# Kernel tuning notes

Hardware: AMD Instinct MI355X
Metric: run time of the kernel (lower is better)

Reference implementation:

```python
import jax, jax.numpy as jnp
import numpy as np

H, W = 4096, 4096
MIN_VAL, MAX_VAL = 0, 256
D = MAX_VAL - MIN_VAL - 1  # 255 candidate thresholds t = 0..254
N_BINS = MAX_VAL           # pixel values live in [0, 256)


def setup_inputs() -> dict:
    key = jax.random.key(0)
    img = jax.random.randint(key, (H, W), MIN_VAL, MAX_VAL, dtype=jnp.int32)
    return {"img_HxW": img}


def reference(img_HxW):
    hw = H * W
    flat = img_HxW.ravel()
    # Histogram of pixel counts and pixel-value sums (float32 accumulation,
    # matching torch.sum(..., dtype=torch.float32) in the original).
    cnt = jax.ops.segment_sum(jnp.ones_like(flat, jnp.float32), flat, num_segments=N_BINS)
    val_sum = jax.ops.segment_sum(flat.astype(jnp.float32), flat, num_segments=N_BINS)
    # Cumulative sums give, for each threshold t, the count/sum of pixels <= t.
    # This equals the original's broadcast compare + masked sum over [H*W, d].
    num_b = jnp.cumsum(cnt)[:D]        # pixels in class "black" (<= t)
    sum_b = jnp.cumsum(val_sum)[:D]    # sum of those pixels
    num_w = hw - num_b                  # pixels in class "white" (> t)
    sum_w = jnp.sum(val_sum) - sum_b
    mean_b = sum_b / num_b
    mean_w = sum_w / num_w
    var_hist = num_b * num_w * (mean_b - mean_w) ** 2  # inter-class variance
    thresh = jnp.argmax(var_hist).astype(jnp.int32)
    bin_img = jnp.where(img_HxW <= thresh,
                        jnp.int32(MIN_VAL), jnp.int32(MAX_VAL))
    return thresh, bin_img
```

## Files before the change

kernel.cpp:

```cpp
#include <hip/hip_runtime.h>

#define HW_TOTAL (4096 * 4096)
#define NBINS 256
#define NCHUNK (HW_TOTAL / 4)
#define HIST_B 512
#define BLK 1024
#define BATCH 8

typedef int int4n __attribute__((ext_vector_type(4)));
typedef int int4a __attribute__((ext_vector_type(4), aligned(4)));

#define WS_NEED (HIST_B * NBINS * 4 + 256)

template <int MODE>
__global__ __launch_bounds__(BLK, 8) void otsu_hist_k(const int4* __restrict__ img4,
                                                      unsigned* __restrict__ out) {
    __shared__ unsigned h[4 * NBINS];
    const int t = threadIdx.x;
    for (int i = t; i < 4 * NBINS; i += BLK) h[i] = 0;
    __syncthreads();

    unsigned* hp = h + (t & 3);
    const int wave = t >> 6, lane = t & 63;
    const int i0 = blockIdx.x * (BLK * BATCH) + wave * (64 * BATCH) + lane;

    int4 v[BATCH];
#pragma unroll
    for (int k = 0; k < BATCH; ++k) v[k] = img4[i0 + k * 64];
#pragma unroll
    for (int k = 0; k < BATCH; ++k) {
        atomicAdd(&hp[((unsigned)v[k].x) << 2], 1u);
        atomicAdd(&hp[((unsigned)v[k].y) << 2], 1u);
        atomicAdd(&hp[((unsigned)v[k].z) << 2], 1u);
        atomicAdd(&hp[((unsigned)v[k].w) << 2], 1u);
    }
    __syncthreads();

    if (t < NBINS) {
        unsigned s = h[t << 2] + h[(t << 2) | 1] + h[(t << 2) | 2] + h[(t << 2) | 3];
        if (MODE == 0) {
            out[blockIdx.x * NBINS + t] = s;
        } else {
            if (s) atomicAdd(&out[t], s);
        }
    }
}

__global__ __launch_bounds__(1024) void otsu_thresh_k(const unsigned* __restrict__ partials,
                                                      int B,
                                                      int* __restrict__ d_out,
                                                      int* __restrict__ thresh_ws) {
    __shared__ unsigned red[4][NBINS];
    __shared__ unsigned cnt[NBINS];

    const int bin = threadIdx.x & 255;
    const int q = threadIdx.x >> 8;
    const int BQ = (B + 3) / 4;
    int r = q * BQ;
    const int e = min((q + 1) * BQ, B);
    unsigned s = 0;
    for (; r + 16 <= e; r += 16) {
#pragma unroll
        for (int k = 0; k < 16; ++k) s += partials[(r + k) * NBINS + bin];
    }
    for (; r < e; ++r) s += partials[r * NBINS + bin];
    red[q][bin] = s;
    __syncthreads();

    if (threadIdx.x < NBINS)
        cnt[bin] = red[0][bin] + red[1][bin] + red[2][bin] + red[3][bin];
    __syncthreads();

    if (threadIdx.x >= 64) return;
    const int lane = threadIdx.x;

    uint4 c4 = ((const uint4*)cnt)[lane];
    unsigned cs[4] = {c4.x, c4.y, c4.z, c4.w};

    unsigned long long lc[4], lv[4];
    unsigned long long ccum = 0ull, vcum = 0ull;
#pragma unroll
    for (int k = 0; k < 4; ++k) {
        ccum += cs[k];
        vcum += (unsigned long long)cs[k] * (unsigned)(4 * lane + k);
        lc[k] = ccum;
        lv[k] = vcum;
    }
    unsigned long long cscan = ccum, vscan = vcum;
    for (int d = 1; d < 64; d <<= 1) {
        unsigned long long cu = __shfl_up(cscan, d);
        unsigned long long vu = __shfl_up(vscan, d);
        if (lane >= d) { cscan += cu; vscan += vu; }
    }
    const unsigned long long cbase = cscan - ccum;
    const unsigned long long vbase = vscan - vcum;
    const unsigned long long vtotal = __shfl(vscan, 63);

    double best = -1.0;
    int bestt = 255;
    const double hw = (double)HW_TOTAL;
    const double vtot_d = (double)vtotal;
#pragma unroll
    for (int k = 0; k < 4; ++k) {
        int tt = 4 * lane + k;
        if (tt > 254) continue;
        double nb = (double)(cbase + lc[k]);
        double sb = (double)(vbase + lv[k]);
        double nw = hw - nb;
        double sw = vtot_d - sb;
        double dm = sb / nb - sw / nw;
        double var = nb * nw * dm * dm;
        if (var > best || (var == best && tt < bestt)) { best = var; bestt = tt; }
    }
    for (int d = 32; d >= 1; d >>= 1) {
        double ov = __shfl_xor(best, d);
        int ot = __shfl_xor(bestt, d);
        if (ov > best || (ov == best && ot < bestt)) { best = ov; bestt = ot; }
    }
    if (lane == 0) {
        d_out[0] = bestt;
        *thresh_ws = bestt;
    }
}

__global__ __launch_bounds__(BLK, 8) void otsu_bin_k(const int* __restrict__ img,
                                                     int* __restrict__ out,
                                                     const int* __restrict__ thresh_ws) {
    const int thresh = *thresh_ws;
    const int t = threadIdx.x;
    const int wave = t >> 6, lane = t & 63;
    const int i0 = blockIdx.x * (BLK * BATCH) + wave * (64 * BATCH) + lane;

#pragma unroll
    for (int k = 0; k < BATCH; ++k) {
        const int c = i0 + k * 64;
        const int4a* vp = (const int4a*)(img + (c ? 4 * c - 1 : 0));
        int4a v = *vp;
        int4n o;
        o.x = (v.x <= thresh) ? 0 : 256;
        o.y = (v.y <= thresh) ? 0 : 256;
        o.z = (v.z <= thresh) ? 0 : 256;
        o.w = (v.w <= thresh) ? 0 : 256;
        if (c == 0) {
            o.w = o.z; o.z = o.y; o.y = o.x; o.x = thresh;
        }
        *((int4n*)out + c) = o;
    }
    if (i0 == 0)
        out[HW_TOTAL] = (img[HW_TOTAL - 1] <= thresh) ? 0 : 256;
}

extern "C" void kernel_launch(void* const* d_in, const int* in_sizes, int n_in,
                              void* d_out, int out_size, void* d_ws, size_t ws_size,
                              hipStream_t stream) {
    const int* img = (const int*)d_in[0];
    int* out = (int*)d_out;
    int* thresh_ws = (int*)d_ws;
    unsigned* hist_buf = (unsigned*)((char*)d_ws + 256);

    if (ws_size >= (size_t)WS_NEED) {
        otsu_hist_k<0><<<HIST_B, BLK, 0, stream>>>((const int4*)img, hist_buf);
        otsu_thresh_k<<<1, 1024, 0, stream>>>(hist_buf, HIST_B, out, thresh_ws);
    } else {
        (void)hipMemsetAsync(hist_buf, 0, NBINS * sizeof(unsigned), stream);
        otsu_hist_k<1><<<HIST_B, BLK, 0, stream>>>((const int4*)img, hist_buf);
        otsu_thresh_k<<<1, 1024, 0, stream>>>(hist_buf, 1, out, thresh_ws);
    }
    otsu_bin_k<<<HIST_B, BLK, 0, stream>>>(img, out, thresh_ws);
}
```

Measured before the change: 44.24 us.

## Fuse histogram, threshold and binarize into one persistent kernel with grid barrier

```diff
diff --git a/kernel.cpp b/kernel.cpp
--- a/kernel.cpp
+++ b/kernel.cpp
@@ -3,88 +3,192 @@
 #define HW_TOTAL (4096 * 4096)
 #define NBINS 256
 #define NCHUNK (HW_TOTAL / 4)
-#define HIST_B 512
+#define GRID_B 256
 #define BLK 1024
-#define BATCH 8
+#define BATCH 16
+#define HALF 8
 
 typedef int int4n __attribute__((ext_vector_type(4)));
 typedef int int4a __attribute__((ext_vector_type(4), aligned(4)));
 
-#define WS_NEED (HIST_B * NBINS * 4 + 256)
-
-template <int MODE>
-__global__ __launch_bounds__(BLK, 8) void otsu_hist_k(const int4* __restrict__ img4,
-                                                      unsigned* __restrict__ out) {
+#define WS_WORDS 258
+#define WS_NEED (WS_WORDS * 4)
+
+__global__ __launch_bounds__(BLK, 4) void otsu_fused_k(const int* __restrict__ img,
+                                                       int* __restrict__ out,
+                                                       unsigned* __restrict__ ws) {
+    __shared__ unsigned h[4 * NBINS];
+    __shared__ int s_thresh;
+    __shared__ unsigned s_islast;
+
+    const int t = threadIdx.x;
+    const int b = blockIdx.x;
+    const int4* img4 = (const int4*)img;
+
+    for (int i = t; i < 4 * NBINS; i += BLK) h[i] = 0;
+    __syncthreads();
+
+    unsigned* hp = h + (t & 3);
+    const int wave = t >> 6, lane = t & 63;
+    const int i0 = b * (BLK * BATCH) + wave * (64 * BATCH) + lane;
+
+#pragma unroll
+    for (int half = 0; half < BATCH / HALF; ++half) {
+        int4 v[HALF];
+        const int j0 = i0 + half * (HALF * 64);
+#pragma unroll
+        for (int k = 0; k < HALF; ++k) v[k] = img4[j0 + k * 64];
+#pragma unroll
+        for (int k = 0; k < HALF; ++k) {
+            atomicAdd(&hp[((unsigned)v[k].x) << 2], 1u);
+            atomicAdd(&hp[((unsigned)v[k].y) << 2], 1u);
+            atomicAdd(&hp[((unsigned)v[k].z) << 2], 1u);
+            atomicAdd(&hp[((unsigned)v[k].w) << 2], 1u);
+        }
+    }
+    __syncthreads();
+
+    if (t < NBINS) {
+        unsigned s = h[t << 2] + h[(t << 2) | 1] + h[(t << 2) | 2] + h[(t << 2) | 3];
+        atomicAdd(&ws[t], s);
+    }
+    __syncthreads();
+
+    if (t == 0) {
+        __threadfence();
+        unsigned my = __hip_atomic_fetch_add(&ws[256], 1u, __ATOMIC_ACQ_REL,
+                                             __HIP_MEMORY_SCOPE_AGENT);
+        s_islast = (my == GRID_B - 1) ? 1u : 0u;
+    }
+    __syncthreads();
+
+    if (s_islast) {
+        if (t < NBINS)
+            h[t] = __hip_atomic_load(&ws[t], __ATOMIC_RELAXED, __HIP_MEMORY_SCOPE_AGENT);
+        __syncthreads();
+        if (t < 64) {
+            uint4 c4 = ((const uint4*)h)[t];
+            unsigned cs[4] = {c4.x, c4.y, c4.z, c4.w};
+
+            unsigned long long lc[4], lv[4];
+            unsigned long long ccum = 0ull, vcum = 0ull;
+#pragma unroll
+            for (int k = 0; k < 4; ++k) {
+                ccum += cs[k];
+                vcum += (unsigned long long)cs[k] * (unsigned)(4 * t + k);
+                lc[k] = ccum;
+                lv[k] = vcum;
+            }
+            unsigned long long cscan = ccum, vscan = vcum;
+            for (int d = 1; d < 64; d <<= 1) {
+                unsigned long long cu = __shfl_up(cscan, d);
+                unsigned long long vu = __shfl_up(vscan, d);
+                if (t >= d) { cscan += cu; vscan += vu; }
+            }
+            const unsigned long long cbase = cscan - ccum;
+            const unsigned long long vbase = vscan - vcum;
+            const unsigned long long vtotal = __shfl(vscan, 63);
+
+            double best = -1.0;
+            int bestt = 255;
+            const double hw = (double)HW_TOTAL;
+            const double vtot_d = (double)vtotal;
+#pragma unroll
+            for (int k = 0; k < 4; ++k) {
+                int tt = 4 * t + k;
+                if (tt > 254) continue;
+                double nb = (double)(cbase + lc[k]);
+                double sb = (double)(vbase + lv[k]);
+                double nw = hw - nb;
+                double sw = vtot_d - sb;
+                double dm = sb / nb - sw / nw;
+                double var = nb * nw * dm * dm;
+                if (var > best || (var == best && tt < bestt)) { best = var; bestt = tt; }
+            }
+            for (int d = 32; d >= 1; d >>= 1) {
+                double ov = __shfl_xor(best, d);
+                int ot = __shfl_xor(bestt, d);
+                if (ov > best || (ov == best && ot < bestt)) { best = ov; bestt = ot; }
+            }
+            if (t == 0) {
+                out[0] = bestt;
+                s_thresh = bestt;
+                __hip_atomic_store(&ws[257], (unsigned)bestt + 1u, __ATOMIC_RELEASE,
+                                   __HIP_MEMORY_SCOPE_AGENT);
+            }
+        }
+    } else if (t == 0) {
+        unsigned f;
+        while ((f = __hip_atomic_load(&ws[257], __ATOMIC_ACQUIRE,
+                                      __HIP_MEMORY_SCOPE_AGENT)) == 0u)
+            __builtin_amdgcn_s_sleep(8);
+        s_thresh = (int)f - 1;
+    }
+    __syncthreads();
+    const int thresh = s_thresh;
+
+#pragma unroll
+    for (int half = 0; half < BATCH / HALF; ++half) {
+        const int j0 = i0 + half * (HALF * 64);
+#pragma unroll
+        for (int k = 0; k < HALF; ++k) {
+            const int c = j0 + k * 64;
+            int4a v = *(const int4a*)(img + (c ? 4 * c - 1 : 0));
+            int4n o;
+            o.x = (v.x <= thresh) ? 0 : 256;
+            o.y = (v.y <= thresh) ? 0 : 256;
+            o.z = (v.z <= thresh) ? 0 : 256;
+            o.w = (v.w <= thresh) ? 0 : 256;
+            if (c == 0) { o.w = o.z; o.z = o.y; o.y = o.x; o.x = thresh; }
+            __builtin_nontemporal_store(o, (int4n*)out + c);
+        }
+    }
+    if (i0 == 0)
+        out[HW_TOTAL] = (img[HW_TOTAL - 1] <= thresh) ? 0 : 256;
+}
+
+__global__ __launch_bounds__(BLK, 4) void fb_hist_k(const int4* __restrict__ img4,
+                                                    unsigned* __restrict__ ghist) {
     __shared__ unsigned h[4 * NBINS];
     const int t = threadIdx.x;
     for (int i = t; i < 4 * NBINS; i += BLK) h[i] = 0;
     __syncthreads();
-
     unsigned* hp = h + (t & 3);
     const int wave = t >> 6, lane = t & 63;
     const int i0 = blockIdx.x * (BLK * BATCH) + wave * (64 * BATCH) + lane;
-
-    int4 v[BATCH];
-#pragma unroll
-    for (int k = 0; k < BATCH; ++k) v[k] = img4[i0 + k * 64];
-#pragma unroll
-    for (int k = 0; k < BATCH; ++k) {
-        atomicAdd(&hp[((unsigned)v[k].x) << 2], 1u);
-        atomicAdd(&hp[((unsigned)v[k].y) << 2], 1u);
-        atomicAdd(&hp[((unsigned)v[k].z) << 2], 1u);
-        atomicAdd(&hp[((unsigned)v[k].w) << 2], 1u);
-    }
-    __syncthreads();
-
+#pragma unroll
+    for (int half = 0; half < BATCH / HALF; ++half) {
+        int4 v[HALF];
+        const int j0 = i0 + half * (HALF * 64);
+#pragma unroll
+        for (int k = 0; k < HALF; ++k) v[k] = img4[j0 + k * 64];
+#pragma unroll
+        for (int k = 0; k < HALF; ++k) {
+            atomicAdd(&hp[((unsigned)v[k].x) << 2], 1u);
+            atomicAdd(&hp[((unsigned)v[k].y) << 2], 1u);
+            atomicAdd(&hp[((unsigned)v[k].z) << 2], 1u);
+            atomicAdd(&hp[((unsigned)v[k].w) << 2], 1u);
+        }
+    }
+    __syncthreads();
     if (t < NBINS) {
         unsigned s = h[t << 2] + h[(t << 2) | 1] + h[(t << 2) | 2] + h[(t << 2) | 3];
-        if (MODE == 0) {
-            out[blockIdx.x * NBINS + t] = s;
-        } else {
-            if (s) atomicAdd(&out[t], s);
-        }
-    }
-}
-
-__global__ __launch_bounds__(1024) void otsu_thresh_k(const unsigned* __restrict__ partials,
-                                                      int B,
-                                                      int* __restrict__ d_out,
-                                                      int* __restrict__ thresh_ws) {
-    __shared__ unsigned red[4][NBINS];
-    __shared__ unsigned cnt[NBINS];
-
-    const int bin = threadIdx.x & 255;
-    const int q = threadIdx.x >> 8;
-    const int BQ = (B + 3) / 4;
-    int r = q * BQ;
-    const int e = min((q + 1) * BQ, B);
-    unsigned s = 0;
-    for (; r + 16 <= e; r += 16) {
-#pragma unroll
-        for (int k = 0; k < 16; ++k) s += partials[(r + k) * NBINS + bin];
-    }
-    for (; r < e; ++r) s += partials[r * NBINS + bin];
-    red[q][bin] = s;
-    __syncthreads();
-
-    if (threadIdx.x < NBINS)
-        cnt[bin] = red[0][bin] + red[1][bin] + red[2][bin] + red[3][bin];
-    __syncthreads();
-
-    if (threadIdx.x >= 64) return;
+        if (s) atomicAdd(&ghist[t], s);
+    }
+}
+
+__global__ __launch_bounds__(64) void fb_thresh_k(const unsigned* __restrict__ cnt,
+                                                  int* __restrict__ d_out,
+                                                  unsigned* __restrict__ ws) {
     const int lane = threadIdx.x;
-
     uint4 c4 = ((const uint4*)cnt)[lane];
     unsigned cs[4] = {c4.x, c4.y, c4.z, c4.w};
-
-    unsigned long long lc[4], lv[4];
-    unsigned long long ccum = 0ull, vcum = 0ull;
+    unsigned long long lc[4], lv[4], ccum = 0ull, vcum = 0ull;
 #pragma unroll
     for (int k = 0; k < 4; ++k) {
         ccum += cs[k];
         vcum += (unsigned long long)cs[k] * (unsigned)(4 * lane + k);
-        lc[k] = ccum;
-        lv[k] = vcum;
+        lc[k] = ccum; lv[k] = vcum;
     }
     unsigned long long cscan = ccum, vscan = vcum;
     for (int d = 1; d < 64; d <<= 1) {
@@ -92,22 +196,15 @@
         unsigned long long vu = __shfl_up(vscan, d);
         if (lane >= d) { cscan += cu; vscan += vu; }
     }
-    const unsigned long long cbase = cscan - ccum;
-    const unsigned long long vbase = vscan - vcum;
+    const unsigned long long cbase = cscan - ccum, vbase = vscan - vcum;
     const unsigned long long vtotal = __shfl(vscan, 63);
-
-    double best = -1.0;
-    int bestt = 255;
-    const double hw = (double)HW_TOTAL;
-    const double vtot_d = (double)vtotal;
+    double best = -1.0; int bestt = 255;
 #pragma unroll
     for (int k = 0; k < 4; ++k) {
         int tt = 4 * lane + k;
         if (tt > 254) continue;
-        double nb = (double)(cbase + lc[k]);
-        double sb = (double)(vbase + lv[k]);
-        double nw = hw - nb;
-        double sw = vtot_d - sb;
+        double nb = (double)(cbase + lc[k]), sb = (double)(vbase + lv[k]);
+        double nw = (double)HW_TOTAL - nb, sw = (double)vtotal - sb;
         double dm = sb / nb - sw / nw;
         double var = nb * nw * dm * dm;
         if (var > best || (var == best && tt < bestt)) { best = var; bestt = tt; }
@@ -117,34 +214,31 @@
         int ot = __shfl_xor(bestt, d);
         if (ov > best || (ov == best && ot < bestt)) { best = ov; bestt = ot; }
     }
-    if (lane == 0) {
-        d_out[0] = bestt;
-        *thresh_ws = bestt;
-    }
-}
-
-__global__ __launch_bounds__(BLK, 8) void otsu_bin_k(const int* __restrict__ img,
-                                                     int* __restrict__ out,
-                                                     const int* __restrict__ thresh_ws) {
-    const int thresh = *thresh_ws;
+    if (lane == 0) { d_out[0] = bestt; ws[257] = (unsigned)bestt + 1u; }
+}
+
+__global__ __launch_bounds__(BLK, 4) void fb_bin_k(const int* __restrict__ img,
+                                                   int* __restrict__ out,
+                                                   const unsigned* __restrict__ ws) {
+    const int thresh = (int)ws[257] - 1;
     const int t = threadIdx.x;
     const int wave = t >> 6, lane = t & 63;
     const int i0 = blockIdx.x * (BLK * BATCH) + wave * (64 * BATCH) + lane;
-
-#pragma unroll
-    for (int k = 0; k < BATCH; ++k) {
-        const int c = i0 + k * 64;
-        const int4a* vp = (const int4a*)(img + (c ? 4 * c - 1 : 0));
-        int4a v = *vp;
-        int4n o;
-        o.x = (v.x <= thresh) ? 0 : 256;
-        o.y = (v.y <= thresh) ? 0 : 256;
-        o.z = (v.z <= thresh) ? 0 : 256;
-        o.w = (v.w <= thresh) ? 0 : 256;
-        if (c == 0) {
-            o.w = o.z; o.z = o.y; o.y = o.x; o.x = thresh;
-        }
-        *((int4n*)out + c) = o;
+#pragma unroll
+    for (int half = 0; half < BATCH / HALF; ++half) {
+        const int j0 = i0 + half * (HALF * 64);
+#pragma unroll
+        for (int k = 0; k < HALF; ++k) {
+            const int c = j0 + k * 64;
+            int4a v = *(const int4a*)(img + (c ? 4 * c - 1 : 0));
+            int4n o;
+            o.x = (v.x <= thresh) ? 0 : 256;
+            o.y = (v.y <= thresh) ? 0 : 256;
+            o.z = (v.z <= thresh) ? 0 : 256;
+            o.w = (v.w <= thresh) ? 0 : 256;
+            if (c == 0) { o.w = o.z; o.z = o.y; o.y = o.x; o.x = thresh; }
+            __builtin_nontemporal_store(o, (int4n*)out + c);
+        }
     }
     if (i0 == 0)
         out[HW_TOTAL] = (img[HW_TOTAL - 1] <= thresh) ? 0 : 256;
@@ -155,16 +249,15 @@
                               hipStream_t stream) {
     const int* img = (const int*)d_in[0];
     int* out = (int*)d_out;
-    int* thresh_ws = (int*)d_ws;
-    unsigned* hist_buf = (unsigned*)((char*)d_ws + 256);
+    unsigned* ws = (unsigned*)d_ws;
+
+    (void)hipMemsetAsync(ws, 0, WS_NEED, stream);
 
     if (ws_size >= (size_t)WS_NEED) {
-        otsu_hist_k<0><<<HIST_B, BLK, 0, stream>>>((const int4*)img, hist_buf);
-        otsu_thresh_k<<<1, 1024, 0, stream>>>(hist_buf, HIST_B, out, thresh_ws);
+        otsu_fused_k<<<GRID_B, BLK, 0, stream>>>(img, out, ws);
     } else {
-        (void)hipMemsetAsync(hist_buf, 0, NBINS * sizeof(unsigned), stream);
-        otsu_hist_k<1><<<HIST_B, BLK, 0, stream>>>((const int4*)img, hist_buf);
-        otsu_thresh_k<<<1, 1024, 0, stream>>>(hist_buf, 1, out, thresh_ws);
-    }
-    otsu_bin_k<<<HIST_B, BLK, 0, stream>>>(img, out, thresh_ws);
-}
+        fb_hist_k<<<GRID_B, BLK, 0, stream>>>((const int4*)img, ws);
+        fb_thresh_k<<<1, 64, 0, stream>>>(ws, out, ws);
+        fb_bin_k<<<GRID_B, BLK, 0, stream>>>(img, out, ws);
+    }
+}
```

Measured after the change: 77.89 us. +76.1%, slower.

## Fuse threshold computation into binarize kernel, use global atomic histogram

Applied to the files above, without the earlier changes.

```diff
diff --git a/kernel.cpp b/kernel.cpp
--- a/kernel.cpp
+++ b/kernel.cpp
@@ -3,77 +3,16 @@
 #define HW_TOTAL (4096 * 4096)
 #define NBINS 256
 #define NCHUNK (HW_TOTAL / 4)
-#define HIST_B 512
+#define GRID_B 512
 #define BLK 1024
 #define BATCH 8
 
 typedef int int4n __attribute__((ext_vector_type(4)));
 typedef int int4a __attribute__((ext_vector_type(4), aligned(4)));
 
-#define WS_NEED (HIST_B * NBINS * 4 + 256)
+#define WS_NEED (NBINS * 4)
 
-template <int MODE>
-__global__ __launch_bounds__(BLK, 8) void otsu_hist_k(const int4* __restrict__ img4,
-                                                      unsigned* __restrict__ out) {
-    __shared__ unsigned h[4 * NBINS];
-    const int t = threadIdx.x;
-    for (int i = t; i < 4 * NBINS; i += BLK) h[i] = 0;
-    __syncthreads();
-
-    unsigned* hp = h + (t & 3);
-    const int wave = t >> 6, lane = t & 63;
-    const int i0 = blockIdx.x * (BLK * BATCH) + wave * (64 * BATCH) + lane;
-
-    int4 v[BATCH];
-#pragma unroll
-    for (int k = 0; k < BATCH; ++k) v[k] = img4[i0 + k * 64];
-#pragma unroll
-    for (int k = 0; k < BATCH; ++k) {
-        atomicAdd(&hp[((unsigned)v[k].x) << 2], 1u);
-        atomicAdd(&hp[((unsigned)v[k].y) << 2], 1u);
-        atomicAdd(&hp[((unsigned)v[k].z) << 2], 1u);
-        atomicAdd(&hp[((unsigned)v[k].w) << 2], 1u);
-    }
-    __syncthreads();
-
-    if (t < NBINS) {
-        unsigned s = h[t << 2] + h[(t << 2) | 1] + h[(t << 2) | 2] + h[(t << 2) | 3];
-        if (MODE == 0) {
-            out[blockIdx.x * NBINS + t] = s;
-        } else {
-            if (s) atomicAdd(&out[t], s);
-        }
-    }
-}
-
-__global__ __launch_bounds__(1024) void otsu_thresh_k(const unsigned* __restrict__ partials,
-                                                      int B,
-                                                      int* __restrict__ d_out,
-                                                      int* __restrict__ thresh_ws) {
-    __shared__ unsigned red[4][NBINS];
-    __shared__ unsigned cnt[NBINS];
-
-    const int bin = threadIdx.x & 255;
-    const int q = threadIdx.x >> 8;
-    const int BQ = (B + 3) / 4;
-    int r = q * BQ;
-    const int e = min((q + 1) * BQ, B);
-    unsigned s = 0;
-    for (; r + 16 <= e; r += 16) {
-#pragma unroll
-        for (int k = 0; k < 16; ++k) s += partials[(r + k) * NBINS + bin];
-    }
-    for (; r < e; ++r) s += partials[r * NBINS + bin];
-    red[q][bin] = s;
-    __syncthreads();
-
-    if (threadIdx.x < NBINS)
-        cnt[bin] = red[0][bin] + red[1][bin] + red[2][bin] + red[3][bin];
-    __syncthreads();
-
-    if (threadIdx.x >= 64) return;
-    const int lane = threadIdx.x;
-
+__device__ __forceinline__ int otsu_scan64(const unsigned* cnt, int lane) {
     uint4 c4 = ((const uint4*)cnt)[lane];
     unsigned cs[4] = {c4.x, c4.y, c4.z, c4.w};
 
@@ -117,34 +56,67 @@
         int ot = __shfl_xor(bestt, d);
         if (ov > best || (ov == best && ot < bestt)) { best = ov; bestt = ot; }
     }
-    if (lane == 0) {
-        d_out[0] = bestt;
-        *thresh_ws = bestt;
+    return bestt;
+}
+
+__global__ __launch_bounds__(BLK, 8) void otsu_hist_k(const int4* __restrict__ img4,
+                                                      unsigned* __restrict__ ghist) {
+    __shared__ unsigned h[4 * NBINS];
+    const int t = threadIdx.x;
+    for (int i = t; i < 4 * NBINS; i += BLK) h[i] = 0;
+    __syncthreads();
+
+    unsigned* hp = h + (t & 3);
+    const int wave = t >> 6, lane = t & 63;
+    const int i0 = blockIdx.x * (BLK * BATCH) + wave * (64 * BATCH) + lane;
+
+    int4 v[BATCH];
+#pragma unroll
+    for (int k = 0; k < BATCH; ++k) v[k] = img4[i0 + k * 64];
+#pragma unroll
+    for (int k = 0; k < BATCH; ++k) {
+        atomicAdd(&hp[((unsigned)v[k].x) << 2], 1u);
+        atomicAdd(&hp[((unsigned)v[k].y) << 2], 1u);
+        atomicAdd(&hp[((unsigned)v[k].z) << 2], 1u);
+        atomicAdd(&hp[((unsigned)v[k].w) << 2], 1u);
+    }
+    __syncthreads();
+
+    if (t < NBINS) {
+        unsigned s = h[t << 2] + h[(t << 2) | 1] + h[(t << 2) | 2] + h[(t << 2) | 3];
+        if (s) atomicAdd(&ghist[t], s);
     }
 }
 
 __global__ __launch_bounds__(BLK, 8) void otsu_bin_k(const int* __restrict__ img,
                                                      int* __restrict__ out,
-                                                     const int* __restrict__ thresh_ws) {
-    const int thresh = *thresh_ws;
+                                                     const unsigned* __restrict__ ghist) {
+    __shared__ unsigned cnt[NBINS];
+    __shared__ int s_thresh;
+
     const int t = threadIdx.x;
+    if (t < NBINS) cnt[t] = ghist[t];
+    __syncthreads();
+    if (t < 64) {
+        int bt = otsu_scan64(cnt, t);
+        if (t == 0) s_thresh = bt;
+    }
+    __syncthreads();
+    const int thresh = s_thresh;
+
     const int wave = t >> 6, lane = t & 63;
     const int i0 = blockIdx.x * (BLK * BATCH) + wave * (64 * BATCH) + lane;
-
 #pragma unroll
     for (int k = 0; k < BATCH; ++k) {
         const int c = i0 + k * 64;
-        const int4a* vp = (const int4a*)(img + (c ? 4 * c - 1 : 0));
-        int4a v = *vp;
+        int4a pv = *(const int4a*)(img + (c ? 4 * c - 1 : 0));
         int4n o;
-        o.x = (v.x <= thresh) ? 0 : 256;
-        o.y = (v.y <= thresh) ? 0 : 256;
-        o.z = (v.z <= thresh) ? 0 : 256;
-        o.w = (v.w <= thresh) ? 0 : 256;
-        if (c == 0) {
-            o.w = o.z; o.z = o.y; o.y = o.x; o.x = thresh;
-        }
-        *((int4n*)out + c) = o;
+        o.x = (pv.x <= thresh) ? 0 : 256;
+        o.y = (pv.y <= thresh) ? 0 : 256;
+        o.z = (pv.z <= thresh) ? 0 : 256;
+        o.w = (pv.w <= thresh) ? 0 : 256;
+        if (c == 0) { o.w = o.z; o.z = o.y; o.y = o.x; o.x = thresh; }
+        __builtin_nontemporal_store(o, (int4n*)out + c);
     }
     if (i0 == 0)
         out[HW_TOTAL] = (img[HW_TOTAL - 1] <= thresh) ? 0 : 256;
@@ -155,16 +127,9 @@
                               hipStream_t stream) {
     const int* img = (const int*)d_in[0];
     int* out = (int*)d_out;
-    int* thresh_ws = (int*)d_ws;
-    unsigned* hist_buf = (unsigned*)((char*)d_ws + 256);
+    unsigned* ghist = (unsigned*)d_ws;
 
-    if (ws_size >= (size_t)WS_NEED) {
-        otsu_hist_k<0><<<HIST_B, BLK, 0, stream>>>((const int4*)img, hist_buf);
-        otsu_thresh_k<<<1, 1024, 0, stream>>>(hist_buf, HIST_B, out, thresh_ws);
-    } else {
-        (void)hipMemsetAsync(hist_buf, 0, NBINS * sizeof(unsigned), stream);
-        otsu_hist_k<1><<<HIST_B, BLK, 0, stream>>>((const int4*)img, hist_buf);
-        otsu_thresh_k<<<1, 1024, 0, stream>>>(hist_buf, 1, out, thresh_ws);
-    }
-    otsu_bin_k<<<HIST_B, BLK, 0, stream>>>(img, out, thresh_ws);
+    (void)hipMemsetAsync(ghist, 0, WS_NEED, stream);
+    otsu_hist_k<<<GRID_B, BLK, 0, stream>>>((const int4*)img, ghist);
+    otsu_bin_k<<<GRID_B, BLK, 0, stream>>>(img, out, ghist);
 }
```

New measurement: 49.41 us. 1.12x slower.
